# Performance work log

Measured on AMD Instinct MI355X. Metric: run time of the kernel, lower is better.

The kernel has to match this reference:

```python
import jax, jax.numpy as jnp
import numpy as np

N_NODES = 100000
N_EDGES = 1600000


def _conv(feat, edge_weight, src, dst, Wp, bp, Wn, bn):
    N = feat.shape[0]
    h = feat @ Wp + bp                              # [N, d_in] pool transform
    m = h[src] * edge_weight[:, None]               # [E, d_in] u_mul_e messages
    neigh = jax.ops.segment_max(m, dst, num_segments=N)
    deg = jax.ops.segment_sum(jnp.ones_like(edge_weight), dst, num_segments=N)
    neigh = jnp.where(deg[:, None] > 0, neigh, 0.0) # zero for in-degree-0 nodes
    return jnp.concatenate([feat, neigh], axis=1) @ Wn + bn


def setup_inputs() -> dict:
    key = jax.random.key(0)
    ks = jax.random.split(key, 20)
    inp = {
        "features": jax.random.uniform(ks[0], (N_NODES, 16), dtype=jnp.float32),
        "edge_weight": jax.random.uniform(ks[1], (N_EDGES,), dtype=jnp.float32),
        "src": jax.random.randint(ks[2], (N_EDGES,), 0, N_NODES, dtype=jnp.int32),
        "dst": jax.random.randint(ks[3], (N_EDGES,), 0, N_NODES, dtype=jnp.int32),
    }
    dims = [16, 48, 48, 1]
    for i in range(3):
        d_in, d_out = dims[i], dims[i + 1]
        inp[f"Wp{i}"] = jax.random.normal(ks[4 + 4 * i], (d_in, d_in), dtype=jnp.float32) * (2.0 / d_in) ** 0.5
        inp[f"bp{i}"] = jnp.zeros((d_in,), dtype=jnp.float32)
        inp[f"Wn{i}"] = jax.random.normal(ks[5 + 4 * i], (2 * d_in, d_out), dtype=jnp.float32) * (1.0 / d_in) ** 0.5
        inp[f"bn{i}"] = jnp.zeros((d_out,), dtype=jnp.float32)
    return inp


def reference(features, edge_weight, src, dst,
              Wp0, bp0, Wn0, bn0, Wp1, bp1, Wn1, bn1, Wp2, bp2, Wn2, bn2):
    params = [(Wp0, bp0, Wn0, bn0), (Wp1, bp1, Wn1, bn1), (Wp2, bp2, Wn2, bn2)]
    h = features
    for (Wp, bp, Wn, bn) in params:
        h = jax.nn.relu(_conv(h, edge_weight, src, dst, Wp, bp, Wn, bn))
    prv_diff = features[:, -2]
    now = features[:, -1]
    delta_ub = jax.ops.segment_sum(prv_diff[src] * edge_weight, dst, num_segments=features.shape[0])
    ub = jnp.clip(now + delta_ub, 0.0, 1.0)
    return jnp.minimum(now + h[:, 0], ub)
```

## Files before the change

### kernel.cpp

```cpp
#include <hip/hip_runtime.h>
#include <hip/hip_fp16.h>
#include <float.h>

#define NN 100000
#define NE 1600000
#define BK 32
#define NB 3125
#define NSUB 8
#define SUBCAP 128
#define BIN_BLOCKS 256
#define BIN_THREADS 1024
#define CHUNK 6250
#define CURPAD 16

__device__ __forceinline__ unsigned encf(float f) {
  unsigned u = __float_as_uint(f);
  return u ^ ((unsigned)((int)u >> 31) | 0x80000000u);
}
__device__ __forceinline__ float decf(unsigned u) {
  return __uint_as_float(u ^ ((u >> 31) ? 0x80000000u : 0xFFFFFFFFu));
}

__device__ __forceinline__ int ntload_i(const int* p) {
  return __builtin_nontemporal_load(p);
}
__device__ __forceinline__ float ntload_f(const float* p) {
  return __builtin_nontemporal_load(p);
}
__device__ __forceinline__ int2 ntload_i2(const int2* p) {
  unsigned long long v = __builtin_nontemporal_load((const unsigned long long*)p);
  int2 r; r.x = (int)(unsigned)(v & 0xFFFFFFFFull); r.y = (int)(unsigned)(v >> 32);
  return r;
}


__global__ void k_zero_int(int* __restrict__ p, int n) {
  int i = blockIdx.x * blockDim.x + threadIdx.x;
  if (i < n) p[i] = 0;
}

__global__ __launch_bounds__(BIN_THREADS)
void k_bin(const int* __restrict__ src, const int* __restrict__ dst,
           const float* __restrict__ ew, int* __restrict__ gcur,
           int2* __restrict__ ebuf) {
  __shared__ int cnt[NB];
  __shared__ int bofs[NB];
  int tid = threadIdx.x;
  int cls = blockIdx.x & 7;
  int e0 = blockIdx.x * CHUNK;
  for (int i = tid; i < NB; i += BIN_THREADS) cnt[i] = 0;
  __syncthreads();
  for (int k = tid; k < CHUNK; k += BIN_THREADS)
    atomicAdd(&cnt[ntload_i(dst + e0 + k) >> 5], 1);
  __syncthreads();
  for (int i = tid; i < NB; i += BIN_THREADS) {
    int c = cnt[i];
    bofs[i] = c ? atomicAdd(&gcur[((i << 3) | cls) * CURPAD], c) : 0;
  }
  __syncthreads();
  for (int i = tid; i < NB; i += BIN_THREADS) cnt[i] = 0;
  __syncthreads();
  for (int k = tid; k < CHUNK; k += BIN_THREADS) {
    int d = ntload_i(dst + e0 + k);
    int b = d >> 5;
    int pos = bofs[b] + atomicAdd(&cnt[b], 1);
    if (pos < SUBCAP)
      ebuf[(size_t)((b << 3) | cls) * SUBCAP + pos] =
          make_int2(ntload_i(src + e0 + k) | ((d & (BK - 1)) << 17),
                    __float_as_int(ntload_f(ew + e0 + k)));
  }
}


__global__ void k_gemm_p16(const float* __restrict__ feat, const float* __restrict__ W,
                           const float* __restrict__ b, __half* __restrict__ out,
                           float2* __restrict__ pv2, int n) {
  __shared__ __align__(16) float sW[256];
  __shared__ float sb[16];
  for (int i = threadIdx.x; i < 256; i += blockDim.x) sW[i] = W[i];
  if (threadIdx.x < 16) sb[threadIdx.x] = b[threadIdx.x];
  __syncthreads();
  int node = blockIdx.x * blockDim.x + threadIdx.x;
  if (node >= n) return;
  float f[16];
  const float4* fr = (const float4*)(feat + (size_t)node * 16);
#pragma unroll
  for (int k = 0; k < 4; k++) {
    float4 t = fr[k];
    f[4 * k] = t.x; f[4 * k + 1] = t.y; f[4 * k + 2] = t.z; f[4 * k + 3] = t.w;
  }
  pv2[node] = make_float2(f[14], f[15]);
  uint2* op = (uint2*)out;
#pragma unroll 1
  for (int j = 0; j < 16; j += 4) {
    float4 acc = *(const float4*)(sb + j);
#pragma unroll
    for (int k = 0; k < 16; k++) {
      float4 w4 = *(const float4*)(sW + k * 16 + j);
      acc.x += f[k] * w4.x; acc.y += f[k] * w4.y;
      acc.z += f[k] * w4.z; acc.w += f[k] * w4.w;
    }
    union { __half2 h2[2]; uint2 u2; } cvt;
    cvt.h2[0] = __floats2half2_rn(acc.x, acc.y);
    cvt.h2[1] = __floats2half2_rn(acc.z, acc.w);
    op[((size_t)node * 16 + j) >> 2] = cvt.u2;
  }
}

__global__ void k_gemm_p48(const float* __restrict__ x, const float* __restrict__ W,
                           const float* __restrict__ b, __half* __restrict__ out, int n) {
  __shared__ __align__(16) float sW[48 * 48];
  __shared__ float sb[48];
  for (int i = threadIdx.x; i < 48 * 48; i += blockDim.x) sW[i] = W[i];
  if (threadIdx.x < 48) sb[threadIdx.x] = b[threadIdx.x];
  __syncthreads();
  int node = blockIdx.x * blockDim.x + threadIdx.x;
  if (node >= n) return;
  float f[48];
  const float4* fr = (const float4*)(x + (size_t)node * 48);
#pragma unroll
  for (int k = 0; k < 12; k++) {
    float4 t = fr[k];
    f[4 * k] = t.x; f[4 * k + 1] = t.y; f[4 * k + 2] = t.z; f[4 * k + 3] = t.w;
  }
  uint2* op = (uint2*)out;
#pragma unroll 1
  for (int j = 0; j < 48; j += 4) {
    float4 acc = *(const float4*)(sb + j);
#pragma unroll
    for (int k = 0; k < 48; k++) {
      float4 w4 = *(const float4*)(sW + k * 48 + j);
      acc.x += f[k] * w4.x; acc.y += f[k] * w4.y;
      acc.z += f[k] * w4.z; acc.w += f[k] * w4.w;
    }
    union { __half2 h2[2]; uint2 u2; } cvt;
    cvt.h2[0] = __floats2half2_rn(acc.x, acc.y);
    cvt.h2[1] = __floats2half2_rn(acc.z, acc.w);
    op[((size_t)node * 48 + j) >> 2] = cvt.u2;
  }
}

template <int DIN>
__global__ void k_gemm_n(const float* __restrict__ feat, const float* __restrict__ neigh,
                         const float* __restrict__ W, const float* __restrict__ b,
                         float* __restrict__ out, int n) {
  constexpr int DOUT = 48;
  constexpr int K = 2 * DIN;
  __shared__ __align__(16) float sW[K * DOUT];
  __shared__ float sb[DOUT];
  for (int i = threadIdx.x; i < K * DOUT; i += blockDim.x) sW[i] = W[i];
  for (int i = threadIdx.x; i < DOUT; i += blockDim.x) sb[i] = b[i];
  __syncthreads();
  int node = blockIdx.x * blockDim.x + threadIdx.x;
  if (node >= n) return;
  float f[K];
  const float4* fr = (const float4*)(feat + (size_t)node * DIN);
#pragma unroll
  for (int k = 0; k < DIN / 4; k++) {
    float4 t = fr[k];
    f[4 * k] = t.x; f[4 * k + 1] = t.y; f[4 * k + 2] = t.z; f[4 * k + 3] = t.w;
  }
  const float4* nr = (const float4*)(neigh + (size_t)node * DIN);
#pragma unroll
  for (int k = 0; k < DIN / 4; k++) {
    float4 t = nr[k];
    f[DIN + 4 * k] = t.x; f[DIN + 4 * k + 1] = t.y;
    f[DIN + 4 * k + 2] = t.z; f[DIN + 4 * k + 3] = t.w;
  }
  float4* op = (float4*)(out + (size_t)node * DOUT);
#pragma unroll 1
  for (int j = 0; j < DOUT; j += 4) {
    float4 acc = *(const float4*)(sb + j);
#pragma unroll
    for (int k = 0; k < K; k++) {
      float4 w4 = *(const float4*)(sW + k * DOUT + j);
      acc.x += f[k] * w4.x; acc.y += f[k] * w4.y;
      acc.z += f[k] * w4.z; acc.w += f[k] * w4.w;
    }
    acc.x = fmaxf(acc.x, 0.f); acc.y = fmaxf(acc.y, 0.f);
    acc.z = fmaxf(acc.z, 0.f); acc.w = fmaxf(acc.w, 0.f);
    op[j / 4] = acc;
  }
}


__global__ __launch_bounds__(128)
void k_seg48(const __half* __restrict__ hp, const int* __restrict__ gcur,
             const int2* __restrict__ ebuf, float* __restrict__ neigh) {
  __shared__ unsigned smax[BK * 49];
  __shared__ int sn[NSUB];
  int tid = threadIdx.x;
  for (int i = tid; i < BK * 49; i += 128) smax[i] = 0u;
  int b = blockIdx.x;
  if (tid < NSUB) {
    int n = gcur[((b << 3) | tid) * CURPAD];
    sn[tid] = n > SUBCAP ? SUBCAP : n;
  }
  __syncthreads();
  int gg = tid >> 4;
  int f = tid & 15;
  const int2* eb = ebuf + (((size_t)b << 3) * SUBCAP);

  for (int win = 0; win < NSUB * SUBCAP; win += 64) {
    int cnt = sn[win >> 7];
    int wpos = win & (SUBCAP - 1);
    if (cnt <= wpos) continue;
    int2 r[8];
#pragma unroll
    for (int k = 0; k < 8; k++) r[k] = ntload_i2(eb + win + gg + 8 * k);
    __half h0[8], h1[8], h2[8];
#pragma unroll
    for (int k = 0; k < 8; k++) {
      int s = (wpos + gg + 8 * k < cnt) ? (r[k].x & 0x1FFFF) : 0;
      const __half* row = hp + (size_t)s * 48 + f;
      h0[k] = row[0]; h1[k] = row[16]; h2[k] = row[32];
    }
#pragma unroll
    for (int k = 0; k < 8; k++) {
      if (wpos + gg + 8 * k < cnt) {
        int dl = (r[k].x >> 17) & (BK - 1);
        float w = __int_as_float(r[k].y);
        unsigned* sm = smax + dl * 49 + f;
        atomicMax(sm,      encf(__half2float(h0[k]) * w));
        atomicMax(sm + 16, encf(__half2float(h1[k]) * w));
        atomicMax(sm + 32, encf(__half2float(h2[k]) * w));
      }
    }
  }
  __syncthreads();
  size_t base = (size_t)b * BK;
  for (int i = tid; i < BK * 48; i += 128) {
    int node = i / 48, ff = i - node * 48;
    unsigned v = smax[node * 49 + ff];
    neigh[base * 48 + i] = v ? decf(v) : 0.0f;
  }
}

__global__ __launch_bounds__(128)
void k_seg16(const __half* __restrict__ hp, const float2* __restrict__ pv2,
             const int* __restrict__ gcur, const int2* __restrict__ ebuf,
             float* __restrict__ neigh, float* __restrict__ delta) {
  __shared__ unsigned smax[BK * 17];
  __shared__ float sdelta[BK];
  __shared__ int sn[NSUB];
  int tid = threadIdx.x;
  for (int i = tid; i < BK * 17; i += 128) smax[i] = 0u;
  if (tid < BK) sdelta[tid] = 0.f;
  int b = blockIdx.x;
  if (tid < NSUB) {
    int n = gcur[((b << 3) | tid) * CURPAD];
    sn[tid] = n > SUBCAP ? SUBCAP : n;
  }
  __syncthreads();
  int gg = tid >> 4;
  int f = tid & 15;
  const int2* eb = ebuf + (((size_t)b << 3) * SUBCAP);

  for (int win = 0; win < NSUB * SUBCAP; win += 64) {
    int cnt = sn[win >> 7];
    int wpos = win & (SUBCAP - 1);
    if (cnt <= wpos) continue;
    int2 r[8];
#pragma unroll
    for (int k = 0; k < 8; k++) r[k] = ntload_i2(eb + win + gg + 8 * k);
    __half h[8];
    float pv[8];
#pragma unroll
    for (int k = 0; k < 8; k++) {
      int s = (wpos + gg + 8 * k < cnt) ? (r[k].x & 0x1FFFF) : 0;
      h[k] = hp[(size_t)s * 16 + f];
      if (f == 0) pv[k] = pv2[s].x;
    }
#pragma unroll
    for (int k = 0; k < 8; k++) {
      if (wpos + gg + 8 * k < cnt) {
        int dl = (r[k].x >> 17) & (BK - 1);
        float w = __int_as_float(r[k].y);
        atomicMax(smax + dl * 17 + f, encf(__half2float(h[k]) * w));
        if (f == 0) atomicAdd(&sdelta[dl], pv[k] * w);
      }
    }
  }
  __syncthreads();
  size_t base = (size_t)b * BK;
  for (int i = tid; i < BK * 16; i += 128) {
    int node = i >> 4;
    unsigned v = smax[node * 17 + (i & 15)];
    neigh[base * 16 + i] = v ? decf(v) : 0.0f;
  }
  if (tid < BK) delta[base + tid] = sdelta[tid];
}


__global__ void k_final(const float* __restrict__ feat48, const float* __restrict__ neigh48,
                        const float* __restrict__ Wn, const float* __restrict__ bn,
                        const float2* __restrict__ pv2, const float* __restrict__ delta,
                        float* __restrict__ out, int n) {
  __shared__ __align__(16) float sW[96];
  __shared__ float sb;
  if (threadIdx.x < 96) sW[threadIdx.x] = Wn[threadIdx.x];
  if (threadIdx.x == 0) sb = bn[0];
  __syncthreads();
  int i = blockIdx.x * blockDim.x + threadIdx.x;
  if (i >= n) return;
  float acc = sb;
  const float4* a = (const float4*)(feat48 + (size_t)i * 48);
#pragma unroll
  for (int k = 0; k < 12; k++) {
    float4 t = a[k];
    acc += t.x * sW[4 * k] + t.y * sW[4 * k + 1] + t.z * sW[4 * k + 2] + t.w * sW[4 * k + 3];
  }
  const float4* b2 = (const float4*)(neigh48 + (size_t)i * 48);
#pragma unroll
  for (int k = 0; k < 12; k++) {
    float4 t = b2[k];
    acc += t.x * sW[48 + 4 * k] + t.y * sW[48 + 4 * k + 1] +
           t.z * sW[48 + 4 * k + 2] + t.w * sW[48 + 4 * k + 3];
  }
  float h = fmaxf(acc, 0.f);
  float2 pn = pv2[i];
  float ub = fminf(fmaxf(pn.y + delta[i], 0.f), 1.f);
  out[i] = fminf(pn.y + h, ub);
}


extern "C" void kernel_launch(void* const* d_in, const int* in_sizes, int n_in,
                              void* d_out, int out_size, void* d_ws, size_t ws_size,
                              hipStream_t stream) {
  const float* features = (const float*)d_in[0];
  const float* ew = (const float*)d_in[1];
  const int* src = (const int*)d_in[2];
  const int* dst = (const int*)d_in[3];
  const float* Wp0 = (const float*)d_in[4];  const float* bp0 = (const float*)d_in[5];
  const float* Wn0 = (const float*)d_in[6];  const float* bn0 = (const float*)d_in[7];
  const float* Wp1 = (const float*)d_in[8];  const float* bp1 = (const float*)d_in[9];
  const float* Wn1 = (const float*)d_in[10]; const float* bn1 = (const float*)d_in[11];
  const float* Wp2 = (const float*)d_in[12]; const float* bp2 = (const float*)d_in[13];
  const float* Wn2 = (const float*)d_in[14]; const float* bn2 = (const float*)d_in[15];
  float* out = (float*)d_out;

  char* base = (char*)d_ws;
  size_t off = 0;
  auto take = [&](size_t bytes) -> void* {
    void* p = base + off;
    off += (bytes + 255) & ~(size_t)255;
    return p;
  };
  __half* H     = (__half*)take((size_t)NN * 48 * 2);
  float*  A     = (float*)take((size_t)NN * 48 * 4);
  float*  X1    = (float*)take((size_t)NN * 48 * 4);
  int*    gcur  = (int*)take((size_t)NB * NSUB * CURPAD * 4);
  int2*   ebuf  = (int2*)take((size_t)NB * NSUB * SUBCAP * 8);
  float*  delta = (float*)take((size_t)NN * 4);
  float2* pv2   = (float2*)take((size_t)NN * 8);
  (void)ws_size; (void)in_sizes; (void)n_in; (void)out_size;

  const int B = 256;
  int nbN = (NN + B - 1) / B;
  int nCur = NB * NSUB * CURPAD;

  k_zero_int<<<(nCur + B - 1) / B, B, 0, stream>>>(gcur, nCur);
  k_bin<<<BIN_BLOCKS, BIN_THREADS, 0, stream>>>(src, dst, ew, gcur, ebuf);

  k_gemm_p16<<<nbN, B, 0, stream>>>(features, Wp0, bp0, H, pv2, NN);
  k_seg16<<<NB, 128, 0, stream>>>(H, pv2, gcur, ebuf, A, delta);
  k_gemm_n<16><<<nbN, B, 0, stream>>>(features, A, Wn0, bn0, X1, NN);

  k_gemm_p48<<<nbN, B, 0, stream>>>(X1, Wp1, bp1, H, NN);
  k_seg48<<<NB, 128, 0, stream>>>(H, gcur, ebuf, A);
  k_gemm_n<48><<<nbN, B, 0, stream>>>(X1, A, Wn1, bn1, X1, NN);

  k_gemm_p48<<<nbN, B, 0, stream>>>(X1, Wp2, bp2, H, NN);
  k_seg48<<<NB, 128, 0, stream>>>(H, gcur, ebuf, A);
  k_final<<<nbN, B, 0, stream>>>(X1, A, Wn2, bn2, pv2, delta, out, NN);
}
```

Baseline: 276.9 us.

## Fuse neighbor-update GEMMs into segment-max kernels for layers 0 and 2

```diff
diff --git a/kernel.cpp b/kernel.cpp
--- a/kernel.cpp
+++ b/kernel.cpp
@@ -140,46 +140,121 @@
   }
 }
 
-template <int DIN>
-__global__ void k_gemm_n(const float* __restrict__ feat, const float* __restrict__ neigh,
-                         const float* __restrict__ W, const float* __restrict__ b,
-                         float* __restrict__ out, int n) {
-  constexpr int DOUT = 48;
-  constexpr int K = 2 * DIN;
-  __shared__ __align__(16) float sW[K * DOUT];
-  __shared__ float sb[DOUT];
-  for (int i = threadIdx.x; i < K * DOUT; i += blockDim.x) sW[i] = W[i];
-  for (int i = threadIdx.x; i < DOUT; i += blockDim.x) sb[i] = b[i];
+__global__ void k_gemm_n48(const float* __restrict__ feat, const float* __restrict__ neigh,
+                           const float* __restrict__ W, const float* __restrict__ b,
+                           float* __restrict__ out, int n) {
+  __shared__ __align__(16) float sW[96 * 48];
+  __shared__ float sb[48];
+  for (int i = threadIdx.x; i < 96 * 48; i += blockDim.x) sW[i] = W[i];
+  if (threadIdx.x < 48) sb[threadIdx.x] = b[threadIdx.x];
   __syncthreads();
   int node = blockIdx.x * blockDim.x + threadIdx.x;
   if (node >= n) return;
-  float f[K];
-  const float4* fr = (const float4*)(feat + (size_t)node * DIN);
-#pragma unroll
-  for (int k = 0; k < DIN / 4; k++) {
+  float f[96];
+  const float4* fr = (const float4*)(feat + (size_t)node * 48);
+#pragma unroll
+  for (int k = 0; k < 12; k++) {
     float4 t = fr[k];
     f[4 * k] = t.x; f[4 * k + 1] = t.y; f[4 * k + 2] = t.z; f[4 * k + 3] = t.w;
   }
-  const float4* nr = (const float4*)(neigh + (size_t)node * DIN);
-#pragma unroll
-  for (int k = 0; k < DIN / 4; k++) {
+  const float4* nr = (const float4*)(neigh + (size_t)node * 48);
+#pragma unroll
+  for (int k = 0; k < 12; k++) {
     float4 t = nr[k];
-    f[DIN + 4 * k] = t.x; f[DIN + 4 * k + 1] = t.y;
-    f[DIN + 4 * k + 2] = t.z; f[DIN + 4 * k + 3] = t.w;
-  }
-  float4* op = (float4*)(out + (size_t)node * DOUT);
+    f[48 + 4 * k] = t.x; f[48 + 4 * k + 1] = t.y;
+    f[48 + 4 * k + 2] = t.z; f[48 + 4 * k + 3] = t.w;
+  }
+  float4* op = (float4*)(out + (size_t)node * 48);
 #pragma unroll 1
-  for (int j = 0; j < DOUT; j += 4) {
+  for (int j = 0; j < 48; j += 4) {
     float4 acc = *(const float4*)(sb + j);
 #pragma unroll
-    for (int k = 0; k < K; k++) {
-      float4 w4 = *(const float4*)(sW + k * DOUT + j);
+    for (int k = 0; k < 96; k++) {
+      float4 w4 = *(const float4*)(sW + k * 48 + j);
       acc.x += f[k] * w4.x; acc.y += f[k] * w4.y;
       acc.z += f[k] * w4.z; acc.w += f[k] * w4.w;
     }
     acc.x = fmaxf(acc.x, 0.f); acc.y = fmaxf(acc.y, 0.f);
     acc.z = fmaxf(acc.z, 0.f); acc.w = fmaxf(acc.w, 0.f);
     op[j / 4] = acc;
+  }
+}
+
+
+__global__ __launch_bounds__(128)
+void k_seg16n(const __half* __restrict__ hp, const float* __restrict__ feat,
+              const float2* __restrict__ pv2, const int* __restrict__ gcur,
+              const int2* __restrict__ ebuf, const float* __restrict__ Wn,
+              const float* __restrict__ bn, float* __restrict__ xout,
+              float* __restrict__ delta) {
+  __shared__ unsigned smax[BK * 17];
+  __shared__ float sdelta[BK];
+  __shared__ int sn[NSUB];
+  __shared__ __align__(16) float sW[32 * 48];
+  __shared__ float sb[48];
+  int tid = threadIdx.x;
+  for (int i = tid; i < BK * 17; i += 128) smax[i] = 0u;
+  if (tid < BK) sdelta[tid] = 0.f;
+  for (int i = tid; i < 32 * 48; i += 128) sW[i] = Wn[i];
+  if (tid < 48) sb[tid] = bn[tid];
+  int b = blockIdx.x;
+  if (tid < NSUB) {
+    int n = gcur[((b << 3) | tid) * CURPAD];
+    sn[tid] = n > SUBCAP ? SUBCAP : n;
+  }
+  __syncthreads();
+  int gg = tid >> 4;
+  int f = tid & 15;
+  const int2* eb = ebuf + (((size_t)b << 3) * SUBCAP);
+
+  for (int win = 0; win < NSUB * SUBCAP; win += 64) {
+    int cnt = sn[win >> 7];
+    int wpos = win & (SUBCAP - 1);
+    if (cnt <= wpos) continue;
+    int2 r[8];
+#pragma unroll
+    for (int k = 0; k < 8; k++) r[k] = ntload_i2(eb + win + gg + 8 * k);
+    __half h[8];
+    float pv[8];
+#pragma unroll
+    for (int k = 0; k < 8; k++) {
+      int s = (wpos + gg + 8 * k < cnt) ? (r[k].x & 0x1FFFF) : 0;
+      h[k] = hp[(size_t)s * 16 + f];
+      if (f == 0) pv[k] = pv2[s].x;
+    }
+#pragma unroll
+    for (int k = 0; k < 8; k++) {
+      if (wpos + gg + 8 * k < cnt) {
+        int dl = (r[k].x >> 17) & (BK - 1);
+        float w = __int_as_float(r[k].y);
+        atomicMax(smax + dl * 17 + f, encf(__half2float(h[k]) * w));
+        if (f == 0) atomicAdd(&sdelta[dl], pv[k] * w);
+      }
+    }
+  }
+  __syncthreads();
+  size_t base = (size_t)b * BK;
+  if (tid < BK) delta[base + tid] = sdelta[tid];
+  int node = tid >> 2;
+  int j0 = (tid & 3) * 12;
+  float fv[32];
+  const float4* fr = (const float4*)(feat + (base + node) * 16);
+#pragma unroll
+  for (int k = 0; k < 4; k++) {
+    float4 t = fr[k];
+    fv[4 * k] = t.x; fv[4 * k + 1] = t.y; fv[4 * k + 2] = t.z; fv[4 * k + 3] = t.w;
+  }
+#pragma unroll
+  for (int k = 0; k < 16; k++) {
+    unsigned v = smax[node * 17 + k];
+    fv[16 + k] = v ? decf(v) : 0.0f;
+  }
+#pragma unroll
+  for (int j = 0; j < 12; j++) {
+    float acc = sb[j0 + j];
+#pragma unroll
+    for (int k = 0; k < 32; k++) acc += fv[k] * sW[k * 48 + j0 + j];
+    xout[(base + node) * 48 + j0 + j] = fmaxf(acc, 0.f);
   }
 }
 
@@ -236,16 +311,21 @@
   }
 }
 
+
 __global__ __launch_bounds__(128)
-void k_seg16(const __half* __restrict__ hp, const float2* __restrict__ pv2,
-             const int* __restrict__ gcur, const int2* __restrict__ ebuf,
-             float* __restrict__ neigh, float* __restrict__ delta) {
-  __shared__ unsigned smax[BK * 17];
-  __shared__ float sdelta[BK];
+void k_seg48f(const __half* __restrict__ hp, const int* __restrict__ gcur,
+              const int2* __restrict__ ebuf, const float* __restrict__ x2,
+              const float* __restrict__ Wn, const float* __restrict__ bn,
+              const float2* __restrict__ pv2, const float* __restrict__ delta,
+              float* __restrict__ out) {
+  __shared__ unsigned smax[BK * 49];
   __shared__ int sn[NSUB];
+  __shared__ __align__(16) float sW[96];
+  __shared__ float sb;
   int tid = threadIdx.x;
-  for (int i = tid; i < BK * 17; i += 128) smax[i] = 0u;
-  if (tid < BK) sdelta[tid] = 0.f;
+  for (int i = tid; i < BK * 49; i += 128) smax[i] = 0u;
+  if (tid < 96) sW[tid] = Wn[tid];
+  if (tid == 0) sb = bn[0];
   int b = blockIdx.x;
   if (tid < NSUB) {
     int n = gcur[((b << 3) | tid) * CURPAD];
@@ -263,64 +343,51 @@
     int2 r[8];
 #pragma unroll
     for (int k = 0; k < 8; k++) r[k] = ntload_i2(eb + win + gg + 8 * k);
-    __half h[8];
-    float pv[8];
+    __half h0[8], h1[8], h2[8];
 #pragma unroll
     for (int k = 0; k < 8; k++) {
       int s = (wpos + gg + 8 * k < cnt) ? (r[k].x & 0x1FFFF) : 0;
-      h[k] = hp[(size_t)s * 16 + f];
-      if (f == 0) pv[k] = pv2[s].x;
+      const __half* row = hp + (size_t)s * 48 + f;
+      h0[k] = row[0]; h1[k] = row[16]; h2[k] = row[32];
     }
 #pragma unroll
     for (int k = 0; k < 8; k++) {
       if (wpos + gg + 8 * k < cnt) {
         int dl = (r[k].x >> 17) & (BK - 1);
         float w = __int_as_float(r[k].y);
-        atomicMax(smax + dl * 17 + f, encf(__half2float(h[k]) * w));
-        if (f == 0) atomicAdd(&sdelta[dl], pv[k] * w);
+        unsigned* sm = smax + dl * 49 + f;
+        atomicMax(sm,      encf(__half2float(h0[k]) * w));
+        atomicMax(sm + 16, encf(__half2float(h1[k]) * w));
+        atomicMax(sm + 32, encf(__half2float(h2[k]) * w));
       }
     }
   }
   __syncthreads();
   size_t base = (size_t)b * BK;
-  for (int i = tid; i < BK * 16; i += 128) {
-    int node = i >> 4;
-    unsigned v = smax[node * 17 + (i & 15)];
-    neigh[base * 16 + i] = v ? decf(v) : 0.0f;
-  }
-  if (tid < BK) delta[base + tid] = sdelta[tid];
-}
-
-
-__global__ void k_final(const float* __restrict__ feat48, const float* __restrict__ neigh48,
-                        const float* __restrict__ Wn, const float* __restrict__ bn,
-                        const float2* __restrict__ pv2, const float* __restrict__ delta,
-                        float* __restrict__ out, int n) {
-  __shared__ __align__(16) float sW[96];
-  __shared__ float sb;
-  if (threadIdx.x < 96) sW[threadIdx.x] = Wn[threadIdx.x];
-  if (threadIdx.x == 0) sb = bn[0];
-  __syncthreads();
-  int i = blockIdx.x * blockDim.x + threadIdx.x;
-  if (i >= n) return;
-  float acc = sb;
-  const float4* a = (const float4*)(feat48 + (size_t)i * 48);
-#pragma unroll
-  for (int k = 0; k < 12; k++) {
-    float4 t = a[k];
-    acc += t.x * sW[4 * k] + t.y * sW[4 * k + 1] + t.z * sW[4 * k + 2] + t.w * sW[4 * k + 3];
-  }
-  const float4* b2 = (const float4*)(neigh48 + (size_t)i * 48);
-#pragma unroll
-  for (int k = 0; k < 12; k++) {
-    float4 t = b2[k];
-    acc += t.x * sW[48 + 4 * k] + t.y * sW[48 + 4 * k + 1] +
-           t.z * sW[48 + 4 * k + 2] + t.w * sW[48 + 4 * k + 3];
-  }
-  float h = fmaxf(acc, 0.f);
-  float2 pn = pv2[i];
-  float ub = fminf(fmaxf(pn.y + delta[i], 0.f), 1.f);
-  out[i] = fminf(pn.y + h, ub);
+  int node = tid >> 2;
+  int part = tid & 3;
+  float acc = 0.f;
+  if (part < 2) {
+    const float* xr = x2 + (base + node) * 48 + part * 24;
+#pragma unroll
+    for (int k = 0; k < 24; k++) acc += xr[k] * sW[part * 24 + k];
+  } else {
+    int k0 = (part - 2) * 24;
+#pragma unroll
+    for (int k = 0; k < 24; k++) {
+      unsigned v = smax[node * 49 + k0 + k];
+      float nv = v ? decf(v) : 0.0f;
+      acc += nv * sW[48 + k0 + k];
+    }
+  }
+  acc += __shfl_xor(acc, 1, 64);
+  acc += __shfl_xor(acc, 2, 64);
+  if (part == 0) {
+    float h = fmaxf(acc + sb, 0.f);
+    float2 pn = pv2[base + node];
+    float ub = fminf(fmaxf(pn.y + delta[base + node], 0.f), 1.f);
+    out[base + node] = fminf(pn.y + h, ub);
+  }
 }
 
 
@@ -363,14 +430,12 @@
   k_bin<<<BIN_BLOCKS, BIN_THREADS, 0, stream>>>(src, dst, ew, gcur, ebuf);
 
   k_gemm_p16<<<nbN, B, 0, stream>>>(features, Wp0, bp0, H, pv2, NN);
-  k_seg16<<<NB, 128, 0, stream>>>(H, pv2, gcur, ebuf, A, delta);
-  k_gemm_n<16><<<nbN, B, 0, stream>>>(features, A, Wn0, bn0, X1, NN);
+  k_seg16n<<<NB, 128, 0, stream>>>(H, features, pv2, gcur, ebuf, Wn0, bn0, X1, delta);
 
   k_gemm_p48<<<nbN, B, 0, stream>>>(X1, Wp1, bp1, H, NN);
   k_seg48<<<NB, 128, 0, stream>>>(H, gcur, ebuf, A);
-  k_gemm_n<48><<<nbN, B, 0, stream>>>(X1, A, Wn1, bn1, X1, NN);
+  k_gemm_n48<<<nbN, B, 0, stream>>>(X1, A, Wn1, bn1, X1, NN);
 
   k_gemm_p48<<<nbN, B, 0, stream>>>(X1, Wp2, bp2, H, NN);
-  k_seg48<<<NB, 128, 0, stream>>>(H, gcur, ebuf, A);
-  k_final<<<nbN, B, 0, stream>>>(X1, A, Wn2, bn2, pv2, delta, out, NN);
-}
+  k_seg48f<<<NB, 128, 0, stream>>>(H, gcur, ebuf, X1, Wn2, bn2, pv2, delta, out);
+}
```

Measured after the change: 260.8 us. -5.8%, faster.
